# Kernel tuning notes

Hardware: AMD Instinct MI355X
Metric: run time of the kernel (lower is better)

Reference implementation:

```python
import jax, jax.numpy as jnp
import numpy as np
import math

IN_FEATURES = 2048
OUT_FEATURES = 8192


def setup_inputs() -> dict:
    key = jax.random.key(0)
    kx, kw = jax.random.split(key)
    x = jax.random.normal(kx, (4, 2048, IN_FEATURES), dtype=jnp.float32)
    stdv = 1.0 / math.sqrt(IN_FEATURES)
    weight = jax.random.uniform(kw, (OUT_FEATURES, IN_FEATURES), dtype=jnp.float32,
                                minval=-stdv, maxval=stdv)
    return {"x": x, "weight": weight}


def reference(x, weight):
    # absmean-based adjustment factor (BitNet b1.58 style)
    scale = 0.0001 + jnp.mean(jnp.abs(weight))
    adjusted = weight / scale
    # two_bit quantization: round then clip to {-1, 0, 1}
    q = jnp.clip(jnp.round(adjusted), -1.0, 1.0)
    # scaled dense matmul: out[b,s,o] = scale * sum_i x[b,s,i] * q[o,i]
    out = scale * jnp.einsum('bsi,oi->bso', x, q)
    return out
```

## Files before the change

### kernel.cpp

```cpp
#include <hip/hip_runtime.h>
#include <hip/hip_bf16.h>


typedef __bf16 bf16x8 __attribute__((ext_vector_type(8)));
typedef float  f32x4  __attribute__((ext_vector_type(4)));

#define GAS __attribute__((address_space(1)))
#define LAS __attribute__((address_space(3)))

static constexpr int  M_DIM = 8192;
static constexpr int  N_DIM = 8192;
static constexpr int  K_DIM = 2048;
static constexpr long NELEM = 16777216;

__global__ void absmean1_kernel(const float* __restrict__ w, double* __restrict__ partials) {
    double s = 0.0;
    const float4* w4 = (const float4*)w;
    const int n4 = (int)(NELEM / 4);
    for (int i = blockIdx.x * blockDim.x + threadIdx.x; i < n4; i += gridDim.x * blockDim.x) {
        float4 v = w4[i];
        s += (double)fabsf(v.x) + (double)fabsf(v.y) + (double)fabsf(v.z) + (double)fabsf(v.w);
    }
    #pragma unroll
    for (int off = 32; off > 0; off >>= 1) s += __shfl_down(s, off);
    __shared__ double wsum[4];
    if ((threadIdx.x & 63) == 0) wsum[threadIdx.x >> 6] = s;
    __syncthreads();
    if (threadIdx.x == 0) partials[blockIdx.x] = wsum[0] + wsum[1] + wsum[2] + wsum[3];
}

__global__ void absmean2_kernel(const double* __restrict__ partials, float* __restrict__ scale_out) {
    double s = 0.0;
    #pragma unroll
    for (int j = 0; j < 8; ++j) s += partials[threadIdx.x + 256 * j];
    #pragma unroll
    for (int off = 32; off > 0; off >>= 1) s += __shfl_down(s, off);
    __shared__ double wsum[4];
    if ((threadIdx.x & 63) == 0) wsum[threadIdx.x >> 6] = s;
    __syncthreads();
    if (threadIdx.x == 0) {
        double total = wsum[0] + wsum[1] + wsum[2] + wsum[3];
        scale_out[0] = (float)(1.0e-4 + total * (1.0 / 16777216.0));
    }
}

__global__ void prep_kernel(const float* __restrict__ x, const float* __restrict__ w,
                            const float* __restrict__ scale_in,
                            __bf16* __restrict__ xs, __bf16* __restrict__ qw) {
    const float scale = scale_in[0];
    const int n8 = (int)(NELEM / 8);
    const float4* x4 = (const float4*)x;
    const float4* w4 = (const float4*)w;
    for (int i = blockIdx.x * blockDim.x + threadIdx.x; i < n8; i += gridDim.x * blockDim.x) {
        float4 a0 = x4[2 * i], a1 = x4[2 * i + 1];
        bf16x8 xv;
        xv[0] = (__bf16)(a0.x * scale); xv[1] = (__bf16)(a0.y * scale);
        xv[2] = (__bf16)(a0.z * scale); xv[3] = (__bf16)(a0.w * scale);
        xv[4] = (__bf16)(a1.x * scale); xv[5] = (__bf16)(a1.y * scale);
        xv[6] = (__bf16)(a1.z * scale); xv[7] = (__bf16)(a1.w * scale);
        *(bf16x8*)(xs + 8l * i) = xv;

        float4 b0 = w4[2 * i], b1 = w4[2 * i + 1];
        float wv[8] = {b0.x, b0.y, b0.z, b0.w, b1.x, b1.y, b1.z, b1.w};
        bf16x8 qv;
        #pragma unroll
        for (int e = 0; e < 8; ++e) {
            float r = rintf(wv[e] / scale);
            r = fminf(1.0f, fmaxf(-1.0f, r));
            qv[e] = (__bf16)r;
        }
        *(bf16x8*)(qw + 8l * i) = qv;
    }
}


#define STAGE_A(dd, t, kt) do { \
    _Pragma("unroll") for (int _h = 0; _h < 2; ++_h) { \
        const __bf16* _g = A + (long)(bm * 256 + _h * 128 + (t) * 64 + (tid >> 3)) * K_DIM \
                             + (kt) * 64 + schunk * 8; \
        __builtin_amdgcn_global_load_lds((const GAS unsigned int*)_g, \
            (LAS unsigned int*)(lds + (dd) * 32768 + _h * 8192 + (t) * 4096 + wid * 512), 16, 0, 0); \
    } } while (0)

#define STAGE_B(dd, h, kt) do { \
    _Pragma("unroll") for (int _t = 0; _t < 2; ++_t) { \
        const __bf16* _g = B + (long)(bn * 256 + (h) * 128 + _t * 64 + (tid >> 3)) * K_DIM \
                             + (kt) * 64 + schunk * 8; \
        __builtin_amdgcn_global_load_lds((const GAS unsigned int*)_g, \
            (LAS unsigned int*)(lds + (dd) * 32768 + 16384 + (h) * 8192 + _t * 4096 + wid * 512), 16, 0, 0); \
    } } while (0)

#define VM2 asm volatile("s_waitcnt vmcnt(2)" ::: "memory")

#define PHASE(dd, mq, nq, STG, DOVM) do { \
    bf16x8 af[4][2], bg[2][2]; \
    _Pragma("unroll") for (int mi = 0; mi < 4; ++mi) \
        _Pragma("unroll") for (int kk = 0; kk < 2; ++kk) \
            af[mi][kk] = *(const bf16x8*)(L + (dd) * 65536 \
                + (wr * 128 + (mq) * 64 + mi * 16 + l15) * 128 + (kk ? kb1 : kb0)); \
    _Pragma("unroll") for (int nj = 0; nj < 2; ++nj) \
        _Pragma("unroll") for (int kk = 0; kk < 2; ++kk) \
            bg[nj][kk] = *(const bf16x8*)(L + (dd) * 65536 + 32768 \
                + (wc * 64 + (nq) * 32 + nj * 16 + l15) * 128 + (kk ? kb1 : kb0)); \
    STG; \
    __builtin_amdgcn_s_barrier(); \
    asm volatile("s_waitcnt lgkmcnt(0)" ::: "memory"); \
    __builtin_amdgcn_sched_barrier(0); \
    __builtin_amdgcn_s_setprio(1); \
    _Pragma("unroll") for (int mi = 0; mi < 4; ++mi) \
        _Pragma("unroll") for (int nj = 0; nj < 2; ++nj) \
            _Pragma("unroll") for (int kk = 0; kk < 2; ++kk) \
                acc[(mq) * 4 + mi][(nq) * 2 + nj] = __builtin_amdgcn_mfma_f32_16x16x32_bf16( \
                    af[mi][kk], bg[nj][kk], acc[(mq) * 4 + mi][(nq) * 2 + nj], 0, 0, 0); \
    __builtin_amdgcn_s_setprio(0); \
    DOVM; \
    __builtin_amdgcn_s_barrier(); \
} while (0)

__global__ __launch_bounds__(512, 2) void gemm_kernel(const __bf16* __restrict__ A,
                                                      const __bf16* __restrict__ B,
                                                      float* __restrict__ C) {
    __shared__ __bf16 lds[65536];

    const int tid  = threadIdx.x;
    const int lane = tid & 63;
    const int wid  = tid >> 6;
    const int wr   = wid >> 2;
    const int wc   = wid & 3;
    const int l15  = lane & 15;

    const int linear = blockIdx.y * gridDim.x + blockIdx.x;
    const int swzid  = (linear & 7) * 128 + (linear >> 3);
    const int bm = swzid >> 5;
    const int bn = swzid & 31;

    const int schunk = (tid & 7) ^ ((tid >> 3) & 7);

    const int swz = (lane & 7) << 4;
    const int khi = ((lane >> 4) & 3) << 4;
    const int kb0 = khi ^ swz;
    const int kb1 = (khi | 64) ^ swz;
    const char* L = (const char*)lds;

    f32x4 acc[8][4];
    #pragma unroll
    for (int i = 0; i < 8; ++i)
        #pragma unroll
        for (int j = 0; j < 4; ++j)
            acc[i][j] = f32x4{0.0f, 0.0f, 0.0f, 0.0f};

    STAGE_A(0, 0, 0);
    STAGE_A(0, 1, 0);
    STAGE_B(0, 0, 0);
    STAGE_B(0, 1, 0);
    STAGE_A(1, 0, 1);
    VM2;
    __builtin_amdgcn_s_barrier();

    const int NITER = K_DIM / 128;
    for (int i = 0; i < NITER; ++i) {
        const int kt1 = 2 * i + 1;
        const int kt2 = (2 * i + 2) & 31;
        const int kt3 = (2 * i + 3) & 31;
        PHASE(0, 0, 0, STAGE_A(1, 1, kt1), );
        PHASE(0, 1, 0, STAGE_B(1, 0, kt1), );
        PHASE(0, 0, 1, STAGE_B(1, 1, kt1), );
        PHASE(0, 1, 1, STAGE_A(0, 0, kt2), VM2);
        PHASE(1, 0, 0, STAGE_B(0, 0, kt2), );
        PHASE(1, 1, 0, STAGE_B(0, 1, kt2), );
        PHASE(1, 0, 1, STAGE_A(0, 1, kt2), );
        PHASE(1, 1, 1, STAGE_A(1, 0, kt3), VM2);
    }

    const int crow = (lane >> 4) << 2;
    #pragma unroll
    for (int mi = 0; mi < 8; ++mi) {
        #pragma unroll
        for (int nj = 0; nj < 4; ++nj) {
            #pragma unroll
            for (int r = 0; r < 4; ++r) {
                const long gm = (long)bm * 256 + wr * 128 + mi * 16 + crow + r;
                const long gn = (long)bn * 256 + wc * 64 + nj * 16 + l15;
                C[gm * N_DIM + gn] = acc[mi][nj][r];
            }
        }
    }
}

extern "C" void kernel_launch(void* const* d_in, const int* in_sizes, int n_in,
                              void* d_out, int out_size, void* d_ws, size_t ws_size,
                              hipStream_t stream) {
    const float* x = (const float*)d_in[0];
    const float* w = (const float*)d_in[1];
    float* out = (float*)d_out;

    char* ws = (char*)d_ws;
    __bf16* qw = (__bf16*)ws;
    __bf16* xs = (__bf16*)(ws + 33554432);

    char* tail = (char*)d_out + (size_t)out_size * sizeof(float);
    double* partials = (double*)(tail - 16384);
    float* scalep    = (float*)(tail - 16448);

    absmean1_kernel<<<2048, 256, 0, stream>>>(w, partials);
    absmean2_kernel<<<1, 256, 0, stream>>>(partials, scalep);
    prep_kernel<<<2048, 256, 0, stream>>>(x, w, scalep, xs, qw);
    dim3 grid(32, 32);
    gemm_kernel<<<grid, 512, 0, stream>>>(xs, qw, out);
}
```

Before: 582.0 us.

## Stage GEMM epilogue through LDS for coalesced float4 stores; reorder prefetch schedule

The epilogue now writes accumulators into a padded LDS tile, one 16-row slice at a time, and then has each thread store contiguous float4 chunks to global memory. This replaces the scattered per-element fp32 stores. The main loop also reorders which A and B sub-tiles are prefetched in each phase and relaxes the vmcnt waits to allow more loads in flight. The cost is extra barriers and LDS traffic in the epilogue, and the reordered waits carry some risk of a hazard if the counts are wrong.

```diff
diff --git a/kernel.cpp b/kernel.cpp
--- a/kernel.cpp
+++ b/kernel.cpp
@@ -91,6 +91,8 @@
     } } while (0)
 
 #define VM2 asm volatile("s_waitcnt vmcnt(2)" ::: "memory")
+#define VM4 asm volatile("s_waitcnt vmcnt(4)" ::: "memory")
+#define VM6 asm volatile("s_waitcnt vmcnt(6)" ::: "memory")
 
 #define PHASE(dd, mq, nq, STG, DOVM) do { \
     bf16x8 af[4][2], bg[2][2]; \
@@ -162,28 +164,40 @@
         const int kt1 = 2 * i + 1;
         const int kt2 = (2 * i + 2) & 31;
         const int kt3 = (2 * i + 3) & 31;
-        PHASE(0, 0, 0, STAGE_A(1, 1, kt1), );
-        PHASE(0, 1, 0, STAGE_B(1, 0, kt1), );
-        PHASE(0, 0, 1, STAGE_B(1, 1, kt1), );
-        PHASE(0, 1, 1, STAGE_A(0, 0, kt2), VM2);
-        PHASE(1, 0, 0, STAGE_B(0, 0, kt2), );
+        PHASE(0, 0, 0, STAGE_B(1, 0, kt1), );
+        PHASE(0, 1, 0, STAGE_B(1, 1, kt1), );
+        PHASE(0, 0, 1, STAGE_A(1, 1, kt1), );
+        PHASE(0, 1, 1, STAGE_A(0, 0, kt2), VM4);
+        PHASE(1, 0, 0, { STAGE_B(0, 0, kt2); STAGE_A(0, 1, kt2); }, VM6);
         PHASE(1, 1, 0, STAGE_B(0, 1, kt2), );
-        PHASE(1, 0, 1, STAGE_A(0, 1, kt2), );
+        PHASE(1, 0, 1, (void)0, );
         PHASE(1, 1, 1, STAGE_A(1, 0, kt3), VM2);
     }
 
-    const int crow = (lane >> 4) << 2;
-    #pragma unroll
+    asm volatile("s_waitcnt vmcnt(0)" ::: "memory");
+    __syncthreads();
+
+    float* ldsF = (float*)lds;
+    const int crow  = (lane >> 4) << 2;
+    const int rho_w = wr * 16 + crow;
+    const int col_w = wc * 64 + l15;
+    const int rho_r = tid >> 4;
+    const int c0    = (tid & 15) << 4;
+    const long gm_r = (long)bm * 256 + (rho_r >> 4) * 128 + (rho_r & 15);
+    const long gn_r = (long)bn * 256 + c0;
+
     for (int mi = 0; mi < 8; ++mi) {
         #pragma unroll
-        for (int nj = 0; nj < 4; ++nj) {
+        for (int nj = 0; nj < 4; ++nj)
             #pragma unroll
-            for (int r = 0; r < 4; ++r) {
-                const long gm = (long)bm * 256 + wr * 128 + mi * 16 + crow + r;
-                const long gn = (long)bn * 256 + wc * 64 + nj * 16 + l15;
-                C[gm * N_DIM + gn] = acc[mi][nj][r];
-            }
-        }
+            for (int r = 0; r < 4; ++r)
+                ldsF[(rho_w + r) * 260 + col_w + nj * 16] = acc[mi][nj][r];
+        __syncthreads();
+        float4* dst = (float4*)(C + (gm_r + (long)mi * 16) * N_DIM + gn_r);
+        const float4* src = (const float4*)(ldsF + rho_r * 260 + c0);
+        #pragma unroll
+        for (int j = 0; j < 4; ++j) dst[j] = src[j];
+        __syncthreads();
     }
 }
 
```

Measured after the change: 633.4 us. +8.8%, slower.
